# Performance work log

Hardware: AMD Instinct MI355X
Metric: run time of the kernel (lower is better)

The kernel has to match this reference:

```python
import jax, jax.numpy as jnp
import numpy as np

N, L, K, D = 16, 1024, 1024, 1024

def setup_inputs() -> dict:
    key = jax.random.key(0)
    k1, k2, k3, k4 = jax.random.split(key, 4)
    scale = 1.0 / np.sqrt(D)
    return {
        "a1": jax.random.normal(k1, (N, L, D), dtype=jnp.float32),
        "a2": jax.random.normal(k2, (N, K, D), dtype=jnp.float32),
        "G_w": jax.random.normal(k3, (D, D), dtype=jnp.float32) * scale,
        "G_b": jax.random.normal(k4, (D,), dtype=jnp.float32) * scale,
    }

def reference(a1, a2, G_w, G_b):
    # Eval mode: LockedDropout is identity. att_type == 0.
    a2p = jnp.einsum('nkd,ed->nke', a2, G_w) + G_b       # G(a2): n,K,d
    S = jnp.einsum('nld,nkd->nlk', a1, a2p)              # score: n,L,K
    A1 = jax.nn.softmax(S, axis=2)                       # over K
    A2 = jax.nn.softmax(S, axis=1)                       # over L
    M1 = jnp.einsum('nlk,nkd->nld', A1, a2)              # n,L,d
    M2 = jnp.einsum('nlk,nld->nkd', A2, a1)              # n,K,d (A2^T @ a1)
    return (M1, M2)
```

## Files before the change

### kernel.cpp

```cpp
#include <hip/hip_runtime.h>
#include <stdint.h>

#define DEVI __device__ __forceinline__

typedef __attribute__((ext_vector_type(4))) float f32x4;
typedef __attribute__((ext_vector_type(8))) short bf16x8;
typedef __attribute__((ext_vector_type(4))) unsigned short u16x4;

DEVI unsigned short f2bf(float x) {
  union { float f; uint32_t u; } v; v.f = x;
  uint32_t r = v.u + 0x7FFFu + ((v.u >> 16) & 1u);
  return (unsigned short)(r >> 16);
}
DEVI float bf2f(unsigned short h) {
  union { uint32_t u; float f; } v; v.u = ((uint32_t)h) << 16;
  return v.f;
}

DEVI void async16(const void* g, void* l) {
  __builtin_amdgcn_global_load_lds((__attribute__((address_space(1))) void*)g,
                                   (__attribute__((address_space(3))) void*)l,
                                   16, 0, 0);
}

__global__ void k_split2(const float* __restrict__ x0, unsigned short* __restrict__ h0,
                         unsigned short* __restrict__ l0,
                         const float* __restrict__ x1, unsigned short* __restrict__ h1,
                         unsigned short* __restrict__ l1) {
  const long i = (long)blockIdx.x * 256 + threadIdx.x;
  const float* x = blockIdx.y ? x1 : x0;
  unsigned short* hh = blockIdx.y ? h1 : h0;
  unsigned short* ll = blockIdx.y ? l1 : l0;
  const f32x4 v = ((const f32x4*)x)[i];
  u16x4 H, L;
#pragma unroll
  for (int j = 0; j < 4; ++j) {
    H[j] = f2bf(v[j]);
    L[j] = f2bf(v[j] - bf2f(H[j]));
  }
  ((u16x4*)hh)[i] = H;
  ((u16x4*)ll)[i] = L;
}

__global__ void k_split(const float* __restrict__ x, unsigned short* __restrict__ hi,
                        unsigned short* __restrict__ lo, const long n4) {
  const long i = (long)blockIdx.x * 256 + threadIdx.x;
  if (i >= n4) return;
  const f32x4 v = ((const f32x4*)x)[i];
  u16x4 H, L;
#pragma unroll
  for (int j = 0; j < 4; ++j) {
    H[j] = f2bf(v[j]);
    L[j] = f2bf(v[j] - bf2f(H[j]));
  }
  ((u16x4*)hi)[i] = H;
  ((u16x4*)lo)[i] = L;
}

template<bool SPLIT, bool OUTSPLIT, bool DUAL>
__global__ __launch_bounds__(512, 2)
void k_gemm256(const unsigned short* __restrict__ Ah, const unsigned short* __restrict__ Al,
               const unsigned short* __restrict__ Bh, const unsigned short* __restrict__ Bl,
               const float* __restrict__ bias,
               float* __restrict__ Cf, unsigned short* __restrict__ Ch,
               unsigned short* __restrict__ Cl,
               const unsigned short* __restrict__ Ax, const unsigned short* __restrict__ Bx,
               float* __restrict__ Cx,
               const int Kd, const int Nn,
               const long sA, const long sB, const long sC,
               const int lgx, const int lgy) {
  __shared__ __align__(16) unsigned short smem[65536];
  const int tid  = threadIdx.x;
  const int lane = tid & 63;
  const int wave = tid >> 6;
  const int wm = wave >> 2, wn = wave & 3;
  const int m16 = lane & 15, quad = lane >> 4;

  const int nper = (int)gridDim.x >> 3;
  const int lin = (int)blockIdx.x;
  const int wg = (lin & 7) * nper + (lin >> 3);
  const int by = wg & ((1 << lgy) - 1);
  const int bx = (wg >> lgy) & ((1 << lgx) - 1);
  int bz = wg >> (lgx + lgy);

  const unsigned short* Ap = Ah;
  const unsigned short* Bp = Bh;
  float* Cp = Cf;
  if (DUAL && bz >= 16) { Ap = Ax; Bp = Bx; Cp = Cx; bz -= 16; }

  const long aTile = (long)bz * sA + (long)bx * 256 * Kd;
  const long bTile = (long)bz * sB + (long)by * 256 * Kd;

  const int row0 = tid >> 2;
  const int kc   = (tid & 3) ^ ((row0 >> 1) & 3);
  const long rstep = 128L * Kd;
  const long aoff = aTile + (long)row0 * Kd + kc * 8;
  const long boff = bTile + (long)row0 * Kd + kc * 8;

  const unsigned short* gA0 = Ap + aoff;
  const unsigned short* gA1 = SPLIT ? (Al + aoff) : (Ap + aoff + 32);
  const unsigned short* gB0 = Bp + boff;
  const unsigned short* gB1 = SPLIT ? (Bl + boff) : (Bp + boff + 32);

  const int ldsW = wave * 512;

  f32x4 acc[8][4];
#pragma unroll
  for (int i = 0; i < 8; ++i)
#pragma unroll
    for (int j = 0; j < 4; ++j) acc[i][j] = (f32x4){0.0f, 0.0f, 0.0f, 0.0f};

  const int KSTEP = SPLIT ? 32 : 64;
  const int NT = Kd / KSTEP;

  async16(gA0,                 smem + ldsW);
  async16(gA0 + rstep,         smem + ldsW + 4096);
  async16(gA1,                 smem + 8192 + ldsW);
  async16(gA1 + rstep,         smem + 8192 + ldsW + 4096);
  async16(gB0,                 smem + 16384 + ldsW);
  async16(gB0 + rstep,         smem + 16384 + ldsW + 4096);
  async16(gB1,                 smem + 24576 + ldsW);
  async16(gB1 + rstep,         smem + 24576 + ldsW + 4096);
  async16(gB0 + KSTEP,         smem + 32768 + 16384 + ldsW);
  async16(gB0 + KSTEP + rstep, smem + 32768 + 16384 + ldsW + 4096);
  async16(gB1 + KSTEP,         smem + 32768 + 24576 + ldsW);
  async16(gB1 + KSTEP + rstep, smem + 32768 + 24576 + ldsW + 4096);
  asm volatile("s_waitcnt vmcnt(4)" ::: "memory");
  asm volatile("s_barrier" ::: "memory");

  const int kx   = (m16 >> 1) & 3;
  const int cp   = quad ^ kx;
  const int aidx = (wm * 128 + m16) * 4 + cp;
  const int bidx = (wn * 64  + m16) * 4 + cp;

#define MFMA_PHASE(q, A0, A1)                                                               \
  {                                                                                         \
    _Pragma("unroll")                                                                       \
    for (int j = 0; j < 2; ++j) {                                                           \
      _Pragma("unroll")                                                                     \
      for (int tn = 0; tn < 4; ++tn) {                                                      \
        acc[2*(q)+j][tn] = __builtin_amdgcn_mfma_f32_16x16x32_bf16(A0[j], b0[tn],           \
                                                                   acc[2*(q)+j][tn], 0,0,0);\
        if (SPLIT) {                                                                        \
          acc[2*(q)+j][tn] = __builtin_amdgcn_mfma_f32_16x16x32_bf16(A0[j], b1[tn],         \
                                                                   acc[2*(q)+j][tn], 0,0,0);\
          acc[2*(q)+j][tn] = __builtin_amdgcn_mfma_f32_16x16x32_bf16(A1[j], b0[tn],         \
                                                                   acc[2*(q)+j][tn], 0,0,0);\
        } else {                                                                            \
          acc[2*(q)+j][tn] = __builtin_amdgcn_mfma_f32_16x16x32_bf16(A1[j], b1[tn],         \
                                                                   acc[2*(q)+j][tn], 0,0,0);\
        }                                                                                   \
      }                                                                                     \
    }                                                                                       \
  }

  for (int i = 0; i < NT; ++i) {
    const int cur = (i & 1) << 15;
    const int nxt = cur ^ 32768;
    const bf16x8* fA0 = (const bf16x8*)(smem + cur);
    const bf16x8* fA1 = (const bf16x8*)(smem + cur + 8192);
    const bf16x8* fB0 = (const bf16x8*)(smem + cur + 16384);
    const bf16x8* fB1 = (const bf16x8*)(smem + cur + 24576);
    const int kA = (i + 1) * KSTEP;
    const int kB = (i + 2) * KSTEP;
    const bool stA = (i + 1 < NT), stB = (i + 2 < NT);

    bf16x8 b0[4], b1[4];
    {
#pragma unroll
      for (int tn = 0; tn < 4; ++tn) {
        b0[tn] = fB0[bidx + tn * 64];
        b1[tn] = fB1[bidx + tn * 64];
      }
      bf16x8 a0[2], a1[2];
      a0[0] = fA0[aidx];      a0[1] = fA0[aidx + 64];
      a1[0] = fA1[aidx];      a1[1] = fA1[aidx + 64];
      if (stA) {
        async16(gA0 + kA,         smem + nxt + ldsW);
        async16(gA0 + kA + rstep, smem + nxt + ldsW + 4096);
      }
      asm volatile("s_waitcnt lgkmcnt(8)" ::: "memory");
      asm volatile("s_barrier" ::: "memory");
      asm volatile("s_waitcnt lgkmcnt(0)" ::: "memory");
      __builtin_amdgcn_sched_barrier(0);
      __builtin_amdgcn_s_setprio(1);
      MFMA_PHASE(0, a0, a1);
      __builtin_amdgcn_s_setprio(0);
      asm volatile("s_barrier" ::: "memory");
    }
    {
      bf16x8 a0[2], a1[2];
      a0[0] = fA0[aidx + 128]; a0[1] = fA0[aidx + 192];
      a1[0] = fA1[aidx + 128]; a1[1] = fA1[aidx + 192];
      if (stA) {
        async16(gA1 + kA,         smem + nxt + 8192 + ldsW);
        async16(gA1 + kA + rstep, smem + nxt + 8192 + ldsW + 4096);
      }
      asm volatile("s_barrier" ::: "memory");
      asm volatile("s_waitcnt lgkmcnt(0)" ::: "memory");
      __builtin_amdgcn_sched_barrier(0);
      __builtin_amdgcn_s_setprio(1);
      MFMA_PHASE(1, a0, a1);
      __builtin_amdgcn_s_setprio(0);
      asm volatile("s_barrier" ::: "memory");
    }
    {
      bf16x8 a0[2], a1[2];
      a0[0] = fA0[aidx + 256]; a0[1] = fA0[aidx + 320];
      a1[0] = fA1[aidx + 256]; a1[1] = fA1[aidx + 320];
      if (stB) {
        async16(gB0 + kB,         smem + cur + 16384 + ldsW);
        async16(gB0 + kB + rstep, smem + cur + 16384 + ldsW + 4096);
      }
      asm volatile("s_barrier" ::: "memory");
      asm volatile("s_waitcnt lgkmcnt(0)" ::: "memory");
      __builtin_amdgcn_sched_barrier(0);
      __builtin_amdgcn_s_setprio(1);
      MFMA_PHASE(2, a0, a1);
      __builtin_amdgcn_s_setprio(0);
      asm volatile("s_barrier" ::: "memory");
    }
    {
      bf16x8 a0[2], a1[2];
      a0[0] = fA0[aidx + 384]; a0[1] = fA0[aidx + 448];
      a1[0] = fA1[aidx + 384]; a1[1] = fA1[aidx + 448];
      if (stB) {
        async16(gB1 + kB,         smem + cur + 24576 + ldsW);
        async16(gB1 + kB + rstep, smem + cur + 24576 + ldsW + 4096);
      }
      asm volatile("s_barrier" ::: "memory");
      asm volatile("s_waitcnt lgkmcnt(0)" ::: "memory");
      __builtin_amdgcn_sched_barrier(0);
      __builtin_amdgcn_s_setprio(1);
      MFMA_PHASE(3, a0, a1);
      __builtin_amdgcn_s_setprio(0);
      if (stB) asm volatile("s_waitcnt vmcnt(4)" ::: "memory");
      else     asm volatile("s_waitcnt vmcnt(0)" ::: "memory");
      asm volatile("s_barrier" ::: "memory");
    }
  }
#undef MFMA_PHASE

  const long crow0 = (long)bx * 256 + wm * 128;
  const long ccol0 = (long)by * 256 + wn * 64;
  const long cBase = (long)bz * sC;
#pragma unroll
  for (int tn = 0; tn < 4; ++tn) {
    const long gcol = ccol0 + tn * 16 + m16;
    const float bv = OUTSPLIT ? bias[gcol] : 0.0f;
#pragma unroll
    for (int tm = 0; tm < 8; ++tm) {
#pragma unroll
      for (int r = 0; r < 4; ++r) {
        const long grow = crow0 + tm * 16 + quad * 4 + r;
        const long idx = cBase + grow * (long)Nn + gcol;
        const float val = acc[tm][tn][r] + bv;
        if (OUTSPLIT) {
          unsigned short h = f2bf(val);
          Ch[idx] = h;
          Cl[idx] = f2bf(val - bf2f(h));
        } else {
          Cp[idx] = val;
        }
      }
    }
  }
}

__global__ void k_rcstats(const float* __restrict__ S, float* __restrict__ m1,
                          float* __restrict__ r1, float* __restrict__ mp,
                          float* __restrict__ sp) {
  if (blockIdx.x < 4096) {
    const int lane = threadIdx.x & 63;
    const int wave = threadIdx.x >> 6;
    const long row = (long)blockIdx.x * 4 + wave;
    const f32x4* p = (const f32x4*)(S + (row << 10));
    f32x4 v[4];
#pragma unroll
    for (int j = 0; j < 4; ++j) v[j] = p[lane + j * 64];
    float mx = -3.4e38f;
#pragma unroll
    for (int j = 0; j < 4; ++j)
#pragma unroll
      for (int c = 0; c < 4; ++c) mx = fmaxf(mx, v[j][c]);
#pragma unroll
    for (int off = 32; off > 0; off >>= 1) mx = fmaxf(mx, __shfl_xor(mx, off, 64));
    float s = 0.0f;
#pragma unroll
    for (int j = 0; j < 4; ++j)
#pragma unroll
      for (int c = 0; c < 4; ++c) s += __expf(v[j][c] - mx);
#pragma unroll
    for (int off = 32; off > 0; off >>= 1) s += __shfl_xor(s, off, 64);
    if (lane == 0) { m1[row] = mx; r1[row] = 1.0f / s; }
  } else {
    const int b = blockIdx.x - 4096;
    const int kc = b & 3, lc = (b >> 2) & 3, n = b >> 4;
    const int k = kc * 256 + threadIdx.x;
    const float* p = S + ((long)n << 20) + ((long)(lc * 256) << 10) + k;
    float m = -3.4e38f, s = 0.0f;
    for (int i = 0; i < 256; ++i) {
      const float x = p[(long)i << 10];
      const float nm = fmaxf(m, x);
      s = s * __expf(m - nm) + __expf(x - nm);
      m = nm;
    }
    const long o = ((long)(n * 4 + lc) << 10) + k;
    mp[o] = m; sp[o] = s;
  }
}

__global__ void k_colstats_comb(const float* __restrict__ mp, const float* __restrict__ sp,
                                float* __restrict__ m2, float* __restrict__ r2) {
  const int n = blockIdx.y;
  const int k = blockIdx.x * 256 + threadIdx.x;
  float m = -3.4e38f, s = 0.0f;
#pragma unroll
  for (int c = 0; c < 4; ++c) {
    const long o = ((long)(n * 4 + c) << 10) + k;
    const float mc = mp[o], sc = sp[o];
    const float nm = fmaxf(m, mc);
    s = s * __expf(m - nm) + sc * __expf(mc - nm);
    m = nm;
  }
  m2[((long)n << 10) + k] = m;
  r2[((long)n << 10) + k] = 1.0f / s;
}

__global__ void k_agen(const float* __restrict__ S, const float* __restrict__ m1,
                       const float* __restrict__ r1, const float* __restrict__ m2,
                       const float* __restrict__ r2, unsigned short* __restrict__ A1,
                       unsigned short* __restrict__ A2T) {
  __shared__ float e2[64][65];
  const int n = blockIdx.z;
  const int k0 = blockIdx.x * 64, l0 = blockIdx.y * 64;
  const int q = threadIdx.x >> 4, p = threadIdx.x & 15;
  const long nb = (long)n << 20;
  const int kk = k0 + p * 4;
  const f32x4 mm2 = *(const f32x4*)(m2 + ((long)n << 10) + kk);
  const f32x4 rr2 = *(const f32x4*)(r2 + ((long)n << 10) + kk);
#pragma unroll
  for (int rr = 0; rr < 4; ++rr) {
    const int lrow = rr * 16 + q;
    const int l = l0 + lrow;
    const f32x4 s4 = *(const f32x4*)(S + nb + ((long)l << 10) + kk);
    const float mv = m1[((long)n << 10) + l], rv = r1[((long)n << 10) + l];
    u16x4 o;
#pragma unroll
    for (int j = 0; j < 4; ++j) {
      o[j] = f2bf(__expf(s4[j] - mv) * rv);
      e2[lrow][p * 4 + j] = __expf(s4[j] - mm2[j]) * rr2[j];
    }
    *(u16x4*)(A1 + nb + ((long)l << 10) + kk) = o;
  }
  __syncthreads();
#pragma unroll
  for (int rr = 0; rr < 4; ++rr) {
    const int krow = rr * 16 + q;
    u16x4 o;
#pragma unroll
    for (int j = 0; j < 4; ++j) o[j] = f2bf(e2[p * 4 + j][krow]);
    *(u16x4*)(A2T + nb + ((long)(k0 + krow) << 10) + (l0 + p * 4)) = o;
  }
}

__global__ void k_transpose2(const float* __restrict__ in0, unsigned short* __restrict__ out0,
                             const float* __restrict__ in1, unsigned short* __restrict__ out1) {
  __shared__ float t[64][65];
  const int zz = blockIdx.z;
  const int n = zz & 15;
  const float* in = (zz < 16) ? in0 : in1;
  unsigned short* out = (zz < 16) ? out0 : out1;
  const int c0 = blockIdx.x * 64, r0 = blockIdx.y * 64;
  const int q = threadIdx.x >> 4, p = threadIdx.x & 15;
  const long nb = (long)n << 20;
#pragma unroll
  for (int rr = 0; rr < 4; ++rr) {
    const int r = rr * 16 + q;
    const f32x4 v = *(const f32x4*)(in + nb + ((long)(r0 + r) << 10) + c0 + p * 4);
#pragma unroll
    for (int j = 0; j < 4; ++j) t[r][p * 4 + j] = v[j];
  }
  __syncthreads();
#pragma unroll
  for (int rr = 0; rr < 4; ++rr) {
    const int c = rr * 16 + q;
    u16x4 o;
#pragma unroll
    for (int j = 0; j < 4; ++j) o[j] = f2bf(t[p * 4 + j][c]);
    *(u16x4*)(out + nb + ((long)(c0 + c) << 10) + (r0 + p * 4)) = o;
  }
}

extern "C" void kernel_launch(void* const* d_in, const int* in_sizes, int n_in,
                              void* d_out, int out_size, void* d_ws, size_t ws_size,
                              hipStream_t stream) {
  const float* a1 = (const float*)d_in[0];
  const float* a2 = (const float*)d_in[1];
  const float* Gw = (const float*)d_in[2];
  const float* Gb = (const float*)d_in[3];
  float* out = (float*)d_out;
  char* ws = (char*)d_ws;
  const size_t MB = 1ull << 20;

  unsigned short* a1h  = (unsigned short*)(ws + 0 * MB);
  unsigned short* a1l  = (unsigned short*)(ws + 32 * MB);
  unsigned short* a2h  = (unsigned short*)(ws + 64 * MB);
  unsigned short* a2l  = (unsigned short*)(ws + 96 * MB);
  unsigned short* a2ph = (unsigned short*)(ws + 128 * MB);
  unsigned short* a2pl = (unsigned short*)(ws + 160 * MB);
  unsigned short* Gh   = (unsigned short*)(ws + 192 * MB);
  unsigned short* Gl   = (unsigned short*)(ws + 194 * MB);
  char* st = ws + 196 * MB;
  float* m1 = (float*)(st);
  float* r1 = (float*)(st + 64 * 1024);
  float* m2 = (float*)(st + 128 * 1024);
  float* r2 = (float*)(st + 192 * 1024);
  float* mp = (float*)(st + 256 * 1024);
  float* sp = (float*)(st + 512 * 1024);
  float* S            = (float*)(ws + 64 * MB);
  unsigned short* A1  = (unsigned short*)(ws + 0 * MB);
  unsigned short* A2T = (unsigned short*)(ws + 32 * MB);
  unsigned short* a2T = (unsigned short*)(ws + 128 * MB);
  unsigned short* a1T = (unsigned short*)(ws + 160 * MB);

  const long B1M = 1048576;

  k_split2<<<dim3(16384, 2), 256, 0, stream>>>(a1, a1h, a1l, a2, a2h, a2l);
  k_split<<<1024, 256, 0, stream>>>(Gw, Gh, Gl, 262144);

  k_gemm256<true, true, false><<<256, 512, 0, stream>>>(
      a2h, a2l, Gh, Gl, Gb, nullptr, a2ph, a2pl, nullptr, nullptr, nullptr,
      1024, 1024, 0, 0, 0, 6, 2);

  k_gemm256<true, false, false><<<256, 512, 0, stream>>>(
      a1h, a1l, a2ph, a2pl, nullptr, S, nullptr, nullptr, nullptr, nullptr, nullptr,
      1024, 1024, B1M, B1M, B1M, 2, 2);

  k_rcstats<<<4352, 256, 0, stream>>>(S, m1, r1, mp, sp);
  k_colstats_comb<<<dim3(4, 16), 256, 0, stream>>>(mp, sp, m2, r2);

  k_agen<<<dim3(16, 16, 16), 256, 0, stream>>>(S, m1, r1, m2, r2, A1, A2T);

  k_transpose2<<<dim3(16, 16, 32), 256, 0, stream>>>(a2, a2T, a1, a1T);

  k_gemm256<false, false, true><<<512, 512, 0, stream>>>(
      A1, nullptr, a2T, nullptr, nullptr, out, nullptr, nullptr,
      A2T, a1T, out + 16777216,
      1024, 1024, B1M, B1M, B1M, 2, 2);
}
```

Before: 602.2 us.

## Triple-buffer A tiles so A and B prefetch two K-steps ahead

Enlarges LDS to hold three A buffers and two B buffers, so A loads are issued two iterations ahead like B instead of one. Each iteration now keeps up to 8 outstanding global-to-LDS loads, and the vmcnt waits are raised to match, giving more time to hide memory latency. The cost is 160KB of LDS per block, which with launch_bounds(512,2) may cut occupancy to one block per CU.

```diff
diff --git a/kernel.cpp b/kernel.cpp
--- a/kernel.cpp
+++ b/kernel.cpp
@@ -69,7 +69,7 @@
                const int Kd, const int Nn,
                const long sA, const long sB, const long sC,
                const int lgx, const int lgy) {
-  __shared__ __align__(16) unsigned short smem[65536];
+  __shared__ __align__(16) unsigned short smem[81920];
   const int tid  = threadIdx.x;
   const int lane = tid & 63;
   const int wave = tid >> 6;
@@ -117,15 +117,19 @@
   async16(gA0 + rstep,         smem + ldsW + 4096);
   async16(gA1,                 smem + 8192 + ldsW);
   async16(gA1 + rstep,         smem + 8192 + ldsW + 4096);
-  async16(gB0,                 smem + 16384 + ldsW);
-  async16(gB0 + rstep,         smem + 16384 + ldsW + 4096);
-  async16(gB1,                 smem + 24576 + ldsW);
-  async16(gB1 + rstep,         smem + 24576 + ldsW + 4096);
-  async16(gB0 + KSTEP,         smem + 32768 + 16384 + ldsW);
-  async16(gB0 + KSTEP + rstep, smem + 32768 + 16384 + ldsW + 4096);
-  async16(gB1 + KSTEP,         smem + 32768 + 24576 + ldsW);
-  async16(gB1 + KSTEP + rstep, smem + 32768 + 24576 + ldsW + 4096);
-  asm volatile("s_waitcnt vmcnt(4)" ::: "memory");
+  async16(gB0,                 smem + 49152 + ldsW);
+  async16(gB0 + rstep,         smem + 49152 + ldsW + 4096);
+  async16(gB1,                 smem + 49152 + 8192 + ldsW);
+  async16(gB1 + rstep,         smem + 49152 + 8192 + ldsW + 4096);
+  async16(gA0 + KSTEP,         smem + 16384 + ldsW);
+  async16(gA0 + KSTEP + rstep, smem + 16384 + ldsW + 4096);
+  async16(gA1 + KSTEP,         smem + 16384 + 8192 + ldsW);
+  async16(gA1 + KSTEP + rstep, smem + 16384 + 8192 + ldsW + 4096);
+  async16(gB0 + KSTEP,         smem + 49152 + 16384 + ldsW);
+  async16(gB0 + KSTEP + rstep, smem + 49152 + 16384 + ldsW + 4096);
+  async16(gB1 + KSTEP,         smem + 49152 + 16384 + 8192 + ldsW);
+  async16(gB1 + KSTEP + rstep, smem + 49152 + 16384 + 8192 + ldsW + 4096);
+  asm volatile("s_waitcnt vmcnt(8)" ::: "memory");
   asm volatile("s_barrier" ::: "memory");
 
   const int kx   = (m16 >> 1) & 3;
@@ -154,16 +158,16 @@
     }                                                                                       \
   }
 
+  int aRd = 0;
   for (int i = 0; i < NT; ++i) {
-    const int cur = (i & 1) << 15;
-    const int nxt = cur ^ 32768;
-    const bf16x8* fA0 = (const bf16x8*)(smem + cur);
-    const bf16x8* fA1 = (const bf16x8*)(smem + cur + 8192);
-    const bf16x8* fB0 = (const bf16x8*)(smem + cur + 16384);
-    const bf16x8* fB1 = (const bf16x8*)(smem + cur + 24576);
-    const int kA = (i + 1) * KSTEP;
-    const int kB = (i + 2) * KSTEP;
-    const bool stA = (i + 1 < NT), stB = (i + 2 < NT);
+    const int aSt = (aRd == 0) ? 32768 : aRd - 16384;
+    const int bB  = 49152 + ((i & 1) << 14);
+    const bf16x8* fA0 = (const bf16x8*)(smem + aRd);
+    const bf16x8* fA1 = (const bf16x8*)(smem + aRd + 8192);
+    const bf16x8* fB0 = (const bf16x8*)(smem + bB);
+    const bf16x8* fB1 = (const bf16x8*)(smem + bB + 8192);
+    const int kN = (i + 2) * KSTEP;
+    const bool st = (i + 2 < NT);
 
     bf16x8 b0[4], b1[4];
     {
@@ -175,9 +179,9 @@
       bf16x8 a0[2], a1[2];
       a0[0] = fA0[aidx];      a0[1] = fA0[aidx + 64];
       a1[0] = fA1[aidx];      a1[1] = fA1[aidx + 64];
-      if (stA) {
-        async16(gA0 + kA,         smem + nxt + ldsW);
-        async16(gA0 + kA + rstep, smem + nxt + ldsW + 4096);
+      if (st) {
+        async16(gA0 + kN,         smem + aSt + ldsW);
+        async16(gA0 + kN + rstep, smem + aSt + ldsW + 4096);
       }
       asm volatile("s_waitcnt lgkmcnt(8)" ::: "memory");
       asm volatile("s_barrier" ::: "memory");
@@ -192,9 +196,9 @@
       bf16x8 a0[2], a1[2];
       a0[0] = fA0[aidx + 128]; a0[1] = fA0[aidx + 192];
       a1[0] = fA1[aidx + 128]; a1[1] = fA1[aidx + 192];
-      if (stA) {
-        async16(gA1 + kA,         smem + nxt + 8192 + ldsW);
-        async16(gA1 + kA + rstep, smem + nxt + 8192 + ldsW + 4096);
+      if (st) {
+        async16(gA1 + kN,         smem + aSt + 8192 + ldsW);
+        async16(gA1 + kN + rstep, smem + aSt + 8192 + ldsW + 4096);
       }
       asm volatile("s_barrier" ::: "memory");
       asm volatile("s_waitcnt lgkmcnt(0)" ::: "memory");
@@ -208,9 +212,9 @@
       bf16x8 a0[2], a1[2];
       a0[0] = fA0[aidx + 256]; a0[1] = fA0[aidx + 320];
       a1[0] = fA1[aidx + 256]; a1[1] = fA1[aidx + 320];
-      if (stB) {
-        async16(gB0 + kB,         smem + cur + 16384 + ldsW);
-        async16(gB0 + kB + rstep, smem + cur + 16384 + ldsW + 4096);
+      if (st) {
+        async16(gB0 + kN,         smem + bB + ldsW);
+        async16(gB0 + kN + rstep, smem + bB + ldsW + 4096);
       }
       asm volatile("s_barrier" ::: "memory");
       asm volatile("s_waitcnt lgkmcnt(0)" ::: "memory");
@@ -224,9 +228,9 @@
       bf16x8 a0[2], a1[2];
       a0[0] = fA0[aidx + 384]; a0[1] = fA0[aidx + 448];
       a1[0] = fA1[aidx + 384]; a1[1] = fA1[aidx + 448];
-      if (stB) {
-        async16(gB1 + kB,         smem + cur + 24576 + ldsW);
-        async16(gB1 + kB + rstep, smem + cur + 24576 + ldsW + 4096);
+      if (st) {
+        async16(gB1 + kN,         smem + bB + 8192 + ldsW);
+        async16(gB1 + kN + rstep, smem + bB + 8192 + ldsW + 4096);
       }
       asm volatile("s_barrier" ::: "memory");
       asm volatile("s_waitcnt lgkmcnt(0)" ::: "memory");
@@ -234,10 +238,11 @@
       __builtin_amdgcn_s_setprio(1);
       MFMA_PHASE(3, a0, a1);
       __builtin_amdgcn_s_setprio(0);
-      if (stB) asm volatile("s_waitcnt vmcnt(4)" ::: "memory");
-      else     asm volatile("s_waitcnt vmcnt(0)" ::: "memory");
-      asm volatile("s_barrier" ::: "memory");
-    }
+      if (st) asm volatile("s_waitcnt vmcnt(8)" ::: "memory");
+      else    asm volatile("s_waitcnt vmcnt(0)" ::: "memory");
+      asm volatile("s_barrier" ::: "memory");
+    }
+    aRd = (aRd == 32768) ? 0 : aRd + 16384;
   }
 #undef MFMA_PHASE
 
```

Result: slower. 614.3 us (+2.0%).
